# Kernel tuning notes

Measured on AMD Instinct MI355X. Metric: run time of the kernel, lower is better.

The kernel has to match this reference:

```python
import jax, jax.numpy as jnp
import numpy as np

N_NODES = 50000

def _gat_conv(x, src, dst, W, a_src, a_dst, bias, num_nodes, concat, neg_slope=0.2):
    # x: [N, Fin]; W: [Fin, H*C]; a_src/a_dst: [H, C]; src/dst: [E]
    H, C = a_src.shape
    h = (x @ W).reshape(-1, H, C)                      # [N, H, C]
    alpha_s = jnp.einsum('nhc,hc->nh', h, a_src)        # [N, H]
    alpha_d = jnp.einsum('nhc,hc->nh', h, a_dst)        # [N, H]
    e = alpha_s[src] + alpha_d[dst]                     # [E, H]
    e = jax.nn.leaky_relu(e, neg_slope)
    # segment softmax over destination nodes
    m = jax.ops.segment_max(e, dst, num_segments=num_nodes)   # [N, H]
    ex = jnp.exp(e - m[dst])                                   # [E, H]
    denom = jax.ops.segment_sum(ex, dst, num_segments=num_nodes)  # [N, H]
    alpha = ex / denom[dst]                                    # [E, H]
    msg = h[src] * alpha[:, :, None]                            # [E, H, C]
    out = jax.ops.segment_sum(msg, dst, num_segments=num_nodes)  # [N, H, C]
    if concat:
        out = out.reshape(-1, H * C)
    else:
        out = out.mean(axis=1)
    return out + bias

def _add_self_loops(edge_index, num_nodes):
    loop = jnp.arange(num_nodes, dtype=edge_index.dtype)
    src = jnp.concatenate([edge_index[0], loop])
    dst = jnp.concatenate([edge_index[1], loop])
    return src, dst

def setup_inputs() -> dict:
    key = jax.random.key(0)
    ks = jax.random.split(key, 12)
    N, E = N_NODES, 800000
    in_c, hid, out_c, H = 128, 32, 64, 4
    x = jax.random.normal(ks[0], (N, in_c), dtype=jnp.float32)
    edge_index = jax.random.randint(ks[1], (2, E), 0, N, dtype=jnp.int64)
    edge_weight = jax.random.uniform(ks[2], (E,), dtype=jnp.float32)
    s1 = 1.0 / np.sqrt(in_c)
    s2 = 1.0 / np.sqrt(hid * H)
    W1 = jax.random.normal(ks[3], (in_c, H * hid), dtype=jnp.float32) * s1
    a_src1 = jax.random.normal(ks[4], (H, hid), dtype=jnp.float32) * s1
    a_dst1 = jax.random.normal(ks[5], (H, hid), dtype=jnp.float32) * s1
    b1 = jnp.zeros((H * hid,), dtype=jnp.float32)
    W2 = jax.random.normal(ks[6], (H * hid, out_c), dtype=jnp.float32) * s2
    a_src2 = jax.random.normal(ks[7], (1, out_c), dtype=jnp.float32) * s2
    a_dst2 = jax.random.normal(ks[8], (1, out_c), dtype=jnp.float32) * s2
    b2 = jnp.zeros((out_c,), dtype=jnp.float32)
    return {"x": x, "edge_index": edge_index, "edge_weight": edge_weight,
            "W1": W1, "a_src1": a_src1, "a_dst1": a_dst1, "b1": b1,
            "W2": W2, "a_src2": a_src2, "a_dst2": a_dst2, "b2": b2}

def reference(x, edge_index, edge_weight, W1, a_src1, a_dst1, b1, W2, a_src2, a_dst2, b2):
    # PyG GATConv with edge_dim unset ignores edge_weight; self-loops added by default
    N = x.shape[0]
    src, dst = _add_self_loops(edge_index, N)
    h = _gat_conv(x, src, dst, W1, a_src1, a_dst1, b1, N, concat=True)
    h = jax.nn.relu(h)
    out = _gat_conv(h, src, dst, W2, a_src2, a_dst2, b2, N, concat=False)
    return out
```

## Files before the change

kernel.cpp:

```cpp
#include <hip/hip_runtime.h>
#include <hip/hip_fp16.h>
#include <math.h>


#define NEG_SLOPE 0.2f
#define NBLKA 256
#define MAXNB 512

__device__ __forceinline__ float leaky(float v) { return v > 0.f ? v : NEG_SLOPE * v; }

__global__ __launch_bounds__(256) void histc_k(const int* __restrict__ ei, int E, int ET,
                                               int* __restrict__ blkpref, int NB) {
  __shared__ int lhist[MAXNB];
  int chunk = (ET + NBLKA - 1) / NBLKA;
  int e0 = blockIdx.x * chunk, e1 = min(ET, e0 + chunk);
  for (int b = threadIdx.x; b < NB; b += 256) lhist[b] = 0;
  __syncthreads();
  for (int e = e0 + threadIdx.x; e < e1; e += 256) {
    int d = (e < E) ? ei[E + e] : (e - E);
    atomicAdd(&lhist[d >> 7], 1);
  }
  __syncthreads();
  for (int b = threadIdx.x; b < NB; b += 256)
    blkpref[b * NBLKA + blockIdx.x] = lhist[b];
}

__global__ __launch_bounds__(256) void scan_blk_k(int* __restrict__ blkpref,
                                                  int* __restrict__ bbase) {
  __shared__ int sm[NBLKA];
  int b = blockIdx.x, t = threadIdx.x;
  int v = blkpref[b * NBLKA + t];
  sm[t] = v;
  __syncthreads();
  #pragma unroll
  for (int off = 1; off < NBLKA; off <<= 1) {
    int x = (t >= off) ? sm[t - off] : 0;
    __syncthreads();
    sm[t] += x;
    __syncthreads();
  }
  blkpref[b * NBLKA + t] = sm[t] - v;
  if (t == NBLKA - 1) bbase[b] = sm[t];
}

__global__ __launch_bounds__(512) void scan_bkt_k(int* __restrict__ bbase,
                                                  int* __restrict__ lcnt,
                                                  int* __restrict__ rowptr,
                                                  int NB, int N, int ET) {
  __shared__ int sm[512];
  int t = threadIdx.x;
  int v = (t < NB) ? bbase[t] : 0;
  sm[t] = v;
  __syncthreads();
  #pragma unroll
  for (int off = 1; off < 512; off <<= 1) {
    int x = (t >= off) ? sm[t - off] : 0;
    __syncthreads();
    sm[t] += x;
    __syncthreads();
  }
  int excl = sm[t] - v;
  if (t <= NB) bbase[t] = excl;
  if (t == 0) { lcnt[0] = 0; lcnt[16] = 0; rowptr[N] = ET; }
}

__global__ __launch_bounds__(256) void passA_k(const int* __restrict__ ei, int E, int ET,
                                               const int* __restrict__ bbase,
                                               const int* __restrict__ blkpref,
                                               int* __restrict__ pairs, int NB) {
  __shared__ int lcur[MAXNB];
  int chunk = (ET + NBLKA - 1) / NBLKA;
  int e0 = blockIdx.x * chunk, e1 = min(ET, e0 + chunk);
  for (int b = threadIdx.x; b < NB; b += 256)
    lcur[b] = bbase[b] + blkpref[b * NBLKA + blockIdx.x];
  __syncthreads();
  for (int e = e0 + threadIdx.x; e < e1; e += 256) {
    int s, d;
    if (e < E) { s = ei[e]; d = ei[E + e]; } else { s = d = e - E; }
    int b = d >> 7;
    int pos = atomicAdd(&lcur[b], 1);
    pairs[pos] = ((d & 127) << 17) | s;
  }
}

__global__ __launch_bounds__(256) void passB_k(const int* __restrict__ pairs,
                                               const int* __restrict__ bbase,
                                               int* __restrict__ rowptr,
                                               int* __restrict__ srcs,
                                               int* __restrict__ small_list,
                                               int* __restrict__ big_list,
                                               int* __restrict__ lcnt, int N) {
  __shared__ int ncnt[128], spre[128], lcur[128];
  __shared__ int wcS[2], wcB[2], bS, bB;
  int b = blockIdx.x, t = threadIdx.x;
  int nb0 = b << 7;
  int nn = min(128, N - nb0);
  int e0 = bbase[b], e1 = bbase[b + 1];
  if (t < 128) ncnt[t] = 0;
  __syncthreads();
  for (int r = e0 + t; r < e1; r += 256)
    atomicAdd(&ncnt[pairs[r] >> 17], 1);
  __syncthreads();
  if (t < 128) spre[t] = ncnt[t];
  __syncthreads();
  #pragma unroll
  for (int off = 1; off < 128; off <<= 1) {
    int x = (t < 128 && t >= off) ? spre[t - off] : 0;
    __syncthreads();
    if (t < 128) spre[t] += x;
    __syncthreads();
  }
  if (t < nn) {
    int base = e0 + spre[t] - ncnt[t];
    rowptr[nb0 + t] = base;
    lcur[t] = base;
  }
  __syncthreads();
  for (int r = e0 + t; r < e1; r += 256) {
    int p = pairs[r];
    int pos = atomicAdd(&lcur[p >> 17], 1);
    srcs[pos] = p & 0x1FFFF;
  }
  int lane = t & 63, wv = t >> 6;
  bool valid = (t < nn);
  int deg = valid ? ncnt[t] : 0;
  bool isS = valid && (deg <= 16);
  bool isB = valid && (deg > 16);
  unsigned long long ms = __ballot(isS);
  unsigned long long mb = __ballot(isB);
  if (lane == 0 && wv < 2) { wcS[wv] = __popcll(ms); wcB[wv] = __popcll(mb); }
  __syncthreads();
  if (t == 0) {
    bS = atomicAdd(&lcnt[0],  wcS[0] + wcS[1]);
    bB = atomicAdd(&lcnt[16], wcB[0] + wcB[1]);
  }
  __syncthreads();
  unsigned long long below = (lane == 0) ? 0ull : (~0ull >> (64 - lane));
  int offS = bS + ((wv == 1) ? wcS[0] : 0);
  int offB = bB + ((wv == 1) ? wcB[0] : 0);
  if (isS) small_list[offS + __popcll(ms & below)] = nb0 + t;
  if (isB) big_list[offB + __popcll(mb & below)]   = nb0 + t;
}

__global__ __launch_bounds__(256) void gemm1_k(const float* __restrict__ X,
                                               const float* __restrict__ W,
                                               const float* __restrict__ aw_s,
                                               const float* __restrict__ aw_d,
                                               __half* __restrict__ Hh,
                                               float* __restrict__ as,
                                               float* __restrict__ ad, int N) {
  __shared__ float wl[32 * 128];
  __shared__ float xt[32][72];
  int cl = threadIdx.x & 31, rg = threadIdx.x >> 5;
  int c4 = cl * 4;
  int n0 = blockIdx.x * 64;
  float acc[8][4] = {};
  const float4* X4 = (const float4*)X;
  const float4* W4 = (const float4*)W;
  for (int k0 = 0; k0 < 128; k0 += 32) {
    __syncthreads();
    for (int i = threadIdx.x; i < 1024; i += 256)
      ((float4*)wl)[i] = W4[k0 * 32 + i];
    for (int i = threadIdx.x; i < 512; i += 256) {
      int r = i >> 3, kk4 = (i & 7) * 4;
      int n = n0 + r;
      float4 xv = (n < N) ? X4[(size_t)n * 32 + (k0 >> 2) + (i & 7)]
                          : make_float4(0.f, 0.f, 0.f, 0.f);
      xt[kk4 + 0][r] = xv.x; xt[kk4 + 1][r] = xv.y;
      xt[kk4 + 2][r] = xv.z; xt[kk4 + 3][r] = xv.w;
    }
    __syncthreads();
    #pragma unroll 8
    for (int kk = 0; kk < 32; ++kk) {
      float4 w4 = *(const float4*)&wl[kk * 128 + c4];
      float4 xa = *(const float4*)&xt[kk][rg * 8];
      float4 xb = *(const float4*)&xt[kk][rg * 8 + 4];
      float xr[8] = {xa.x, xa.y, xa.z, xa.w, xb.x, xb.y, xb.z, xb.w};
      #pragma unroll
      for (int j = 0; j < 8; ++j) {
        acc[j][0] += xr[j] * w4.x; acc[j][1] += xr[j] * w4.y;
        acc[j][2] += xr[j] * w4.z; acc[j][3] += xr[j] * w4.w;
      }
    }
  }
  float4 aws = *(const float4*)&aw_s[c4];
  float4 awd = *(const float4*)&aw_d[c4];
  #pragma unroll
  for (int j = 0; j < 8; ++j) {
    int n = n0 + rg * 8 + j;
    float ps = acc[j][0] * aws.x + acc[j][1] * aws.y + acc[j][2] * aws.z + acc[j][3] * aws.w;
    float pd = acc[j][0] * awd.x + acc[j][1] * awd.y + acc[j][2] * awd.z + acc[j][3] * awd.w;
    ps += __shfl_xor(ps, 1); ps += __shfl_xor(ps, 2); ps += __shfl_xor(ps, 4);
    pd += __shfl_xor(pd, 1); pd += __shfl_xor(pd, 2); pd += __shfl_xor(pd, 4);
    if (n < N) {
      __half2* dst = (__half2*)&Hh[(size_t)n * 128 + c4];
      dst[0] = __floats2half2_rn(acc[j][0], acc[j][1]);
      dst[1] = __floats2half2_rn(acc[j][2], acc[j][3]);
      if ((cl & 7) == 0) {
        as[n * 4 + (cl >> 3)] = ps;
        ad[n * 4 + (cl >> 3)] = pd;
      }
    }
  }
}

__global__ __launch_bounds__(256) void gemm2_k(const __half* __restrict__ X,
                                               const float* __restrict__ W,
                                               const float* __restrict__ aw_s,
                                               const float* __restrict__ aw_d,
                                               __half* __restrict__ Hh,
                                               float* __restrict__ as,
                                               float* __restrict__ ad, int N) {
  __shared__ float wl[32 * 64];
  __shared__ float xt[32][72];
  int cl = threadIdx.x & 15, rg = threadIdx.x >> 4;
  int c4 = cl * 4;
  int n0 = blockIdx.x * 64;
  float acc[4][4] = {};
  const uint4* X8 = (const uint4*)X;
  const float4* W4 = (const float4*)W;
  for (int k0 = 0; k0 < 128; k0 += 32) {
    __syncthreads();
    for (int i = threadIdx.x; i < 512; i += 256)
      ((float4*)wl)[i] = W4[k0 * 16 + i];
    for (int i = threadIdx.x; i < 256; i += 256) {
      int r = i >> 2, kk8 = (i & 3) * 8;
      int n = n0 + r;
      uint4 hv = (n < N) ? X8[(size_t)n * 16 + (k0 >> 3) + (i & 3)]
                         : make_uint4(0, 0, 0, 0);
      float2 f0 = __half22float2(*(const __half2*)&hv.x);
      float2 f1 = __half22float2(*(const __half2*)&hv.y);
      float2 f2 = __half22float2(*(const __half2*)&hv.z);
      float2 f3 = __half22float2(*(const __half2*)&hv.w);
      xt[kk8 + 0][r] = f0.x; xt[kk8 + 1][r] = f0.y;
      xt[kk8 + 2][r] = f1.x; xt[kk8 + 3][r] = f1.y;
      xt[kk8 + 4][r] = f2.x; xt[kk8 + 5][r] = f2.y;
      xt[kk8 + 6][r] = f3.x; xt[kk8 + 7][r] = f3.y;
    }
    __syncthreads();
    #pragma unroll 8
    for (int kk = 0; kk < 32; ++kk) {
      float4 w4 = *(const float4*)&wl[kk * 64 + c4];
      float4 xa = *(const float4*)&xt[kk][rg * 4];
      float xr[4] = {xa.x, xa.y, xa.z, xa.w};
      #pragma unroll
      for (int j = 0; j < 4; ++j) {
        acc[j][0] += xr[j] * w4.x; acc[j][1] += xr[j] * w4.y;
        acc[j][2] += xr[j] * w4.z; acc[j][3] += xr[j] * w4.w;
      }
    }
  }
  float4 aws = *(const float4*)&aw_s[c4];
  float4 awd = *(const float4*)&aw_d[c4];
  #pragma unroll
  for (int j = 0; j < 4; ++j) {
    int n = n0 + rg * 4 + j;
    float ps = acc[j][0] * aws.x + acc[j][1] * aws.y + acc[j][2] * aws.z + acc[j][3] * aws.w;
    float pd = acc[j][0] * awd.x + acc[j][1] * awd.y + acc[j][2] * awd.z + acc[j][3] * awd.w;
    ps += __shfl_xor(ps, 1); ps += __shfl_xor(ps, 2);
    ps += __shfl_xor(ps, 4); ps += __shfl_xor(ps, 8);
    pd += __shfl_xor(pd, 1); pd += __shfl_xor(pd, 2);
    pd += __shfl_xor(pd, 4); pd += __shfl_xor(pd, 8);
    if (n < N) {
      __half2* dst = (__half2*)&Hh[(size_t)n * 64 + c4];
      dst[0] = __floats2half2_rn(acc[j][0], acc[j][1]);
      dst[1] = __floats2half2_rn(acc[j][2], acc[j][3]);
      if (cl == 0) { as[n] = ps; ad[n] = pd; }
    }
  }
}

__device__ __forceinline__ void load8h(const __half* p, float* f) {
  uint4 hv = *(const uint4*)p;
  float2 f0 = __half22float2(*(const __half2*)&hv.x);
  float2 f1 = __half22float2(*(const __half2*)&hv.y);
  float2 f2 = __half22float2(*(const __half2*)&hv.z);
  float2 f3 = __half22float2(*(const __half2*)&hv.w);
  f[0] = f0.x; f[1] = f0.y; f[2] = f1.x; f[3] = f1.y;
  f[4] = f2.x; f[5] = f2.y; f[6] = f3.x; f[7] = f3.y;
}

__global__ __launch_bounds__(256) void agg1_k(const int* __restrict__ rowptr,
                                              const int* __restrict__ srcs,
                                              const float* __restrict__ as,
                                              const float* __restrict__ ad,
                                              const __half* __restrict__ Hm,
                                              const float* __restrict__ bias,
                                              __half* __restrict__ out,
                                              const int* __restrict__ small_list,
                                              const int* __restrict__ big_list,
                                              const int* __restrict__ lcnt, int SB) {
  if (blockIdx.x < (unsigned)SB) {
    __shared__ float al_sm[16][17][4];
    __shared__ int   sr_sm[16][16];
    int g  = threadIdx.x >> 4;
    int gl = threadIdx.x & 15;
    int gidx = blockIdx.x * 16 + g;
    if (gidx >= lcnt[0]) return;
    int n = small_list[gidx];
    int r0 = rowptr[n];
    int deg = rowptr[n + 1] - r0;
    float4 adn = *(const float4*)&ad[n * 4];

    float e0 = -INFINITY, e1 = -INFINITY, e2 = -INFINITY, e3 = -INFINITY;
    int s = 0;
    if (gl < deg) {
      s = srcs[r0 + gl];
      float4 av = *(const float4*)&as[s * 4];
      e0 = leaky(av.x + adn.x); e1 = leaky(av.y + adn.y);
      e2 = leaky(av.z + adn.z); e3 = leaky(av.w + adn.w);
    }
    sr_sm[g][gl] = s;
    float m0 = e0, m1 = e1, m2 = e2, m3 = e3;
    #pragma unroll
    for (int off = 8; off > 0; off >>= 1) {
      m0 = fmaxf(m0, __shfl_xor(m0, off, 16)); m1 = fmaxf(m1, __shfl_xor(m1, off, 16));
      m2 = fmaxf(m2, __shfl_xor(m2, off, 16)); m3 = fmaxf(m3, __shfl_xor(m3, off, 16));
    }
    float sc0 = (gl < deg) ? __expf(e0 - m0) : 0.f;
    float sc1 = (gl < deg) ? __expf(e1 - m1) : 0.f;
    float sc2 = (gl < deg) ? __expf(e2 - m2) : 0.f;
    float sc3 = (gl < deg) ? __expf(e3 - m3) : 0.f;
    float s0 = sc0, s1 = sc1, s2 = sc2, s3 = sc3;
    #pragma unroll
    for (int off = 8; off > 0; off >>= 1) {
      s0 += __shfl_xor(s0, off, 16); s1 += __shfl_xor(s1, off, 16);
      s2 += __shfl_xor(s2, off, 16); s3 += __shfl_xor(s3, off, 16);
    }
    *(float4*)&al_sm[g][gl][0] =
        make_float4(sc0 / s0, sc1 / s1, sc2 / s2, sc3 / s3);

    int h = gl >> 2;
    int cbase = gl * 8;
    float a0 = 0.f, a1 = 0.f, a2 = 0.f, a3 = 0.f,
          a4 = 0.f, a5 = 0.f, a6 = 0.f, a7 = 0.f;
    for (int j = 0; j < deg; j += 4) {
      #pragma unroll
      for (int u = 0; u < 4; ++u) {
        int idx = j + u;
        bool vU = idx < deg;
        int jj = vU ? idx : 0;
        int   sU  = sr_sm[g][jj];
        float alU = vU ? al_sm[g][jj][h] : 0.f;
        float f[8];
        load8h(&Hm[(size_t)sU * 128 + cbase], f);
        a0 += f[0] * alU; a1 += f[1] * alU; a2 += f[2] * alU; a3 += f[3] * alU;
        a4 += f[4] * alU; a5 += f[5] * alU; a6 += f[6] * alU; a7 += f[7] * alU;
      }
    }
    float4 b0 = *(const float4*)&bias[cbase];
    float4 b1 = *(const float4*)&bias[cbase + 4];
    __half2* dst = (__half2*)&out[(size_t)n * 128 + cbase];
    dst[0] = __floats2half2_rn(fmaxf(a0 + b0.x, 0.f), fmaxf(a1 + b0.y, 0.f));
    dst[1] = __floats2half2_rn(fmaxf(a2 + b0.z, 0.f), fmaxf(a3 + b0.w, 0.f));
    dst[2] = __floats2half2_rn(fmaxf(a4 + b1.x, 0.f), fmaxf(a5 + b1.y, 0.f));
    dst[3] = __floats2half2_rn(fmaxf(a6 + b1.z, 0.f), fmaxf(a7 + b1.w, 0.f));
    return;
  }
  __shared__ float al_sm[4][64][4];
  __shared__ int   sr_sm[4][64];
  int wv = threadIdx.x >> 6, lane = threadIdx.x & 63;
  int widx = (blockIdx.x - SB) * 4 + wv;
  if (widx >= lcnt[16]) return;
  int n = big_list[widx];
  int r0 = rowptr[n], r1 = rowptr[n + 1];
  int deg = r1 - r0;
  int grp = lane >> 4, gl = lane & 15, h = gl >> 2;
  int cbase = gl * 8;
  float4 adn = *(const float4*)&ad[n * 4];

  float a0 = 0.f, a1 = 0.f, a2 = 0.f, a3 = 0.f,
        a4 = 0.f, a5 = 0.f, a6 = 0.f, a7 = 0.f;

  if (deg <= 64) {
    float e0 = -INFINITY, e1 = -INFINITY, e2 = -INFINITY, e3 = -INFINITY;
    int s = 0;
    if (lane < deg) {
      s = srcs[r0 + lane];
      float4 av = *(const float4*)&as[s * 4];
      e0 = leaky(av.x + adn.x); e1 = leaky(av.y + adn.y);
      e2 = leaky(av.z + adn.z); e3 = leaky(av.w + adn.w);
    }
    sr_sm[wv][lane] = s;
    float m0 = e0, m1 = e1, m2 = e2, m3 = e3;
    #pragma unroll
    for (int off = 32; off > 0; off >>= 1) {
      m0 = fmaxf(m0, __shfl_xor(m0, off)); m1 = fmaxf(m1, __shfl_xor(m1, off));
      m2 = fmaxf(m2, __shfl_xor(m2, off)); m3 = fmaxf(m3, __shfl_xor(m3, off));
    }
    float sc0 = (lane < deg) ? __expf(e0 - m0) : 0.f;
    float sc1 = (lane < deg) ? __expf(e1 - m1) : 0.f;
    float sc2 = (lane < deg) ? __expf(e2 - m2) : 0.f;
    float sc3 = (lane < deg) ? __expf(e3 - m3) : 0.f;
    float s0 = sc0, s1 = sc1, s2 = sc2, s3 = sc3;
    #pragma unroll
    for (int off = 32; off > 0; off >>= 1) {
      s0 += __shfl_xor(s0, off); s1 += __shfl_xor(s1, off);
      s2 += __shfl_xor(s2, off); s3 += __shfl_xor(s3, off);
    }
    *(float4*)&al_sm[wv][lane][0] =
        make_float4(sc0 / s0, sc1 / s1, sc2 / s2, sc3 / s3);

    for (int base = 0; base < deg; base += 16) {
      #pragma unroll
      for (int u = 0; u < 4; ++u) {
        int idx = base + grp * 4 + u;
        bool vU = idx < deg;
        int jj = vU ? idx : 0;
        int   sU  = sr_sm[wv][jj];
        float alU = vU ? al_sm[wv][jj][h] : 0.f;
        float f[8];
        load8h(&Hm[(size_t)sU * 128 + cbase], f);
        a0 += f[0] * alU; a1 += f[1] * alU; a2 += f[2] * alU; a3 += f[3] * alU;
        a4 += f[4] * alU; a5 += f[5] * alU; a6 += f[6] * alU; a7 += f[7] * alU;
      }
    }
  } else {
    float m0 = -INFINITY, m1 = -INFINITY, m2 = -INFINITY, m3 = -INFINITY;
    for (int r = r0 + lane; r < r1; r += 64) {
      int s = srcs[r];
      float4 av = *(const float4*)&as[s * 4];
      m0 = fmaxf(m0, leaky(av.x + adn.x)); m1 = fmaxf(m1, leaky(av.y + adn.y));
      m2 = fmaxf(m2, leaky(av.z + adn.z)); m3 = fmaxf(m3, leaky(av.w + adn.w));
    }
    #pragma unroll
    for (int off = 32; off > 0; off >>= 1) {
      m0 = fmaxf(m0, __shfl_xor(m0, off)); m1 = fmaxf(m1, __shfl_xor(m1, off));
      m2 = fmaxf(m2, __shfl_xor(m2, off)); m3 = fmaxf(m3, __shfl_xor(m3, off));
    }
    float s0 = 0.f, s1 = 0.f, s2 = 0.f, s3 = 0.f;
    for (int r = r0 + lane; r < r1; r += 64) {
      int s = srcs[r];
      float4 av = *(const float4*)&as[s * 4];
      s0 += __expf(leaky(av.x + adn.x) - m0); s1 += __expf(leaky(av.y + adn.y) - m1);
      s2 += __expf(leaky(av.z + adn.z) - m2); s3 += __expf(leaky(av.w + adn.w) - m3);
    }
    #pragma unroll
    for (int off = 32; off > 0; off >>= 1) {
      s0 += __shfl_xor(s0, off); s1 += __shfl_xor(s1, off);
      s2 += __shfl_xor(s2, off); s3 += __shfl_xor(s3, off);
    }
    float mhh = (h == 0) ? m0 : (h == 1) ? m1 : (h == 2) ? m2 : m3;
    float inv = 1.f / ((h == 0) ? s0 : (h == 1) ? s1 : (h == 2) ? s2 : s3);
    float adh = (h == 0) ? adn.x : (h == 1) ? adn.y : (h == 2) ? adn.z : adn.w;
    for (int r = r0; r < r1; r += 8) {
      int rA = r + grp, rB = rA + 4;
      bool vA = rA < r1, vB = rB < r1;
      int sA = srcs[vA ? rA : r0];
      int sB = srcs[vB ? rB : r0];
      float avA = as[sA * 4 + h], avB = as[sB * 4 + h];
      float alA = vA ? (__expf(leaky(avA + adh) - mhh) * inv) : 0.f;
      float alB = vB ? (__expf(leaky(avB + adh) - mhh) * inv) : 0.f;
      float fA[8], fB[8];
      load8h(&Hm[(size_t)sA * 128 + cbase], fA);
      load8h(&Hm[(size_t)sB * 128 + cbase], fB);
      a0 += fA[0] * alA + fB[0] * alB; a1 += fA[1] * alA + fB[1] * alB;
      a2 += fA[2] * alA + fB[2] * alB; a3 += fA[3] * alA + fB[3] * alB;
      a4 += fA[4] * alA + fB[4] * alB; a5 += fA[5] * alA + fB[5] * alB;
      a6 += fA[6] * alA + fB[6] * alB; a7 += fA[7] * alA + fB[7] * alB;
    }
  }
  a0 += __shfl_xor(a0, 16); a0 += __shfl_xor(a0, 32);
  a1 += __shfl_xor(a1, 16); a1 += __shfl_xor(a1, 32);
  a2 += __shfl_xor(a2, 16); a2 += __shfl_xor(a2, 32);
  a3 += __shfl_xor(a3, 16); a3 += __shfl_xor(a3, 32);
  a4 += __shfl_xor(a4, 16); a4 += __shfl_xor(a4, 32);
  a5 += __shfl_xor(a5, 16); a5 += __shfl_xor(a5, 32);
  a6 += __shfl_xor(a6, 16); a6 += __shfl_xor(a6, 32);
  a7 += __shfl_xor(a7, 16); a7 += __shfl_xor(a7, 32);
  if (grp == 0) {
    float4 b0 = *(const float4*)&bias[cbase];
    float4 b1 = *(const float4*)&bias[cbase + 4];
    __half2* dst = (__half2*)&out[(size_t)n * 128 + cbase];
    dst[0] = __floats2half2_rn(fmaxf(a0 + b0.x, 0.f), fmaxf(a1 + b0.y, 0.f));
    dst[1] = __floats2half2_rn(fmaxf(a2 + b0.z, 0.f), fmaxf(a3 + b0.w, 0.f));
    dst[2] = __floats2half2_rn(fmaxf(a4 + b1.x, 0.f), fmaxf(a5 + b1.y, 0.f));
    dst[3] = __floats2half2_rn(fmaxf(a6 + b1.z, 0.f), fmaxf(a7 + b1.w, 0.f));
  }
}

__global__ __launch_bounds__(256) void agg2_k(const int* __restrict__ rowptr,
                                              const int* __restrict__ srcs,
                                              const float* __restrict__ as,
                                              const float* __restrict__ ad,
                                              const __half* __restrict__ Hm,
                                              const float* __restrict__ bias,
                                              float* __restrict__ out,
                                              const int* __restrict__ small_list,
                                              const int* __restrict__ big_list,
                                              const int* __restrict__ lcnt, int SB) {
  if (blockIdx.x < (unsigned)SB) {
    __shared__ float al_sm[16][17];
    __shared__ int   sr_sm[16][16];
    int g  = threadIdx.x >> 4;
    int gl = threadIdx.x & 15;
    int gidx = blockIdx.x * 16 + g;
    if (gidx >= lcnt[0]) return;
    int n = small_list[gidx];
    int r0 = rowptr[n];
    int deg = rowptr[n + 1] - r0;
    float adn = ad[n];

    float e = -INFINITY;
    int s = 0;
    if (gl < deg) { s = srcs[r0 + gl]; e = leaky(as[s] + adn); }
    sr_sm[g][gl] = s;
    float m = e;
    #pragma unroll
    for (int off = 8; off > 0; off >>= 1) m = fmaxf(m, __shfl_xor(m, off, 16));
    float sc = (gl < deg) ? __expf(e - m) : 0.f;
    float ssum = sc;
    #pragma unroll
    for (int off = 8; off > 0; off >>= 1) ssum += __shfl_xor(ssum, off, 16);
    al_sm[g][gl] = sc / ssum;

    int cbase = gl * 4;
    float a0 = 0.f, a1 = 0.f, a2 = 0.f, a3 = 0.f;
    for (int j = 0; j < deg; j += 4) {
      #pragma unroll
      for (int u = 0; u < 4; ++u) {
        int idx = j + u;
        bool vU = idx < deg;
        int jj = vU ? idx : 0;
        int   sU  = sr_sm[g][jj];
        float alU = vU ? al_sm[g][jj] : 0.f;
        uint2 hv = *(const uint2*)&Hm[(size_t)sU * 64 + cbase];
        float2 f0 = __half22float2(*(const __half2*)&hv.x);
        float2 f1 = __half22float2(*(const __half2*)&hv.y);
        a0 += f0.x * alU; a1 += f0.y * alU; a2 += f1.x * alU; a3 += f1.y * alU;
      }
    }
    float4 bv = *(const float4*)&bias[cbase];
    float4 o;
    o.x = a0 + bv.x; o.y = a1 + bv.y; o.z = a2 + bv.z; o.w = a3 + bv.w;
    *(float4*)&out[(size_t)n * 64 + cbase] = o;
    return;
  }
  __shared__ float al_sm[4][64];
  __shared__ int   sr_sm[4][64];
  int wv = threadIdx.x >> 6, lane = threadIdx.x & 63;
  int widx = (blockIdx.x - SB) * 4 + wv;
  if (widx >= lcnt[16]) return;
  int n = big_list[widx];
  int r0 = rowptr[n], r1 = rowptr[n + 1];
  int deg = r1 - r0;
  int grp = lane >> 4, gl = lane & 15;
  int cbase = gl * 4;
  float adn = ad[n];

  float a0 = 0.f, a1 = 0.f, a2 = 0.f, a3 = 0.f;

  if (deg <= 64) {
    float e = -INFINITY;
    int s = 0;
    if (lane < deg) { s = srcs[r0 + lane]; e = leaky(as[s] + adn); }
    sr_sm[wv][lane] = s;
    float m = e;
    #pragma unroll
    for (int off = 32; off > 0; off >>= 1) m = fmaxf(m, __shfl_xor(m, off));
    float sc = (lane < deg) ? __expf(e - m) : 0.f;
    float ssum = sc;
    #pragma unroll
    for (int off = 32; off > 0; off >>= 1) ssum += __shfl_xor(ssum, off);
    al_sm[wv][lane] = sc / ssum;

    for (int base = 0; base < deg; base += 16) {
      #pragma unroll
      for (int u = 0; u < 4; ++u) {
        int idx = base + grp * 4 + u;
        bool vU = idx < deg;
        int jj = vU ? idx : 0;
        int   sU  = sr_sm[wv][jj];
        float alU = vU ? al_sm[wv][jj] : 0.f;
        uint2 hv = *(const uint2*)&Hm[(size_t)sU * 64 + cbase];
        float2 f0 = __half22float2(*(const __half2*)&hv.x);
        float2 f1 = __half22float2(*(const __half2*)&hv.y);
        a0 += f0.x * alU; a1 += f0.y * alU; a2 += f1.x * alU; a3 += f1.y * alU;
      }
    }
  } else {
    float mh = -INFINITY;
    for (int r = r0 + lane; r < r1; r += 64)
      mh = fmaxf(mh, leaky(as[srcs[r]] + adn));
    #pragma unroll
    for (int off = 32; off > 0; off >>= 1) mh = fmaxf(mh, __shfl_xor(mh, off));
    float ssum = 0.f;
    for (int r = r0 + lane; r < r1; r += 64)
      ssum += __expf(leaky(as[srcs[r]] + adn) - mh);
    #pragma unroll
    for (int off = 32; off > 0; off >>= 1) ssum += __shfl_xor(ssum, off);
    float inv = 1.f / ssum;
    for (int r = r0; r < r1; r += 8) {
      int rA = r + grp, rB = rA + 4;
      bool vA = rA < r1, vB = rB < r1;
      int sA = srcs[vA ? rA : r0];
      int sB = srcs[vB ? rB : r0];
      float alA = vA ? (__expf(leaky(as[sA] + adn) - mh) * inv) : 0.f;
      float alB = vB ? (__expf(leaky(as[sB] + adn) - mh) * inv) : 0.f;
      uint2 hvA = *(const uint2*)&Hm[(size_t)sA * 64 + cbase];
      uint2 hvB = *(const uint2*)&Hm[(size_t)sB * 64 + cbase];
      float2 fA0 = __half22float2(*(const __half2*)&hvA.x);
      float2 fA1 = __half22float2(*(const __half2*)&hvA.y);
      float2 fB0 = __half22float2(*(const __half2*)&hvB.x);
      float2 fB1 = __half22float2(*(const __half2*)&hvB.y);
      a0 += fA0.x * alA + fB0.x * alB; a1 += fA0.y * alA + fB0.y * alB;
      a2 += fA1.x * alA + fB1.x * alB; a3 += fA1.y * alA + fB1.y * alB;
    }
  }
  a0 += __shfl_xor(a0, 16); a0 += __shfl_xor(a0, 32);
  a1 += __shfl_xor(a1, 16); a1 += __shfl_xor(a1, 32);
  a2 += __shfl_xor(a2, 16); a2 += __shfl_xor(a2, 32);
  a3 += __shfl_xor(a3, 16); a3 += __shfl_xor(a3, 32);
  if (grp == 0) {
    float4 bv = *(const float4*)&bias[cbase];
    float4 o;
    o.x = a0 + bv.x; o.y = a1 + bv.y; o.z = a2 + bv.z; o.w = a3 + bv.w;
    *(float4*)&out[(size_t)n * 64 + cbase] = o;
  }
}

extern "C" void kernel_launch(void* const* d_in, const int* in_sizes, int n_in,
                              void* d_out, int out_size, void* d_ws, size_t ws_size,
                              hipStream_t stream) {
  const float* x   = (const float*)d_in[0];
  const int*   ei  = (const int*)d_in[1];
  const float* W1  = (const float*)d_in[3];
  const float* aS1 = (const float*)d_in[4];
  const float* aD1 = (const float*)d_in[5];
  const float* b1  = (const float*)d_in[6];
  const float* W2  = (const float*)d_in[7];
  const float* aS2 = (const float*)d_in[8];
  const float* aD2 = (const float*)d_in[9];
  const float* b2  = (const float*)d_in[10];

  const int N  = in_sizes[0] / 128;
  const int E  = in_sizes[2];
  const int ET = E + N;
  const int NB = (N + 127) >> 7;

  float* ws    = (float*)d_ws;
  __half* h1h  = (__half*)ws;
  __half* o1h  = (__half*)(ws + (size_t)N * 64);
  float* as1   = ws + (size_t)N * 128;
  float* ad1   = as1  + (size_t)4 * N;
  float* as2   = ad1  + (size_t)4 * N;
  float* ad2   = as2  + (size_t)N;
  int*   lcnt    = (int*)(ad2 + (size_t)N);
  int*   rowptr  = lcnt + 32;
  int*   bbase   = rowptr + N + 1;
  int*   blkpref = bbase + NB + 1;
  int*   small_list = blkpref + NB * NBLKA;
  int*   big_list   = small_list + N;
  int*   srcs   = big_list + N;
  int*   pairs  = (int*)ws;
  __half* h2h  = h1h;
  float* out  = (float*)d_out;

  const int gb = (N + 63) / 64;
  const int sb = (N + 15) / 16;
  const int bb = (N + 3) / 4;

  histc_k<<<NBLKA, 256, 0, stream>>>(ei, E, ET, blkpref, NB);
  scan_blk_k<<<NB, 256, 0, stream>>>(blkpref, bbase);
  scan_bkt_k<<<1, 512, 0, stream>>>(bbase, lcnt, rowptr, NB, N, ET);
  passA_k<<<NBLKA, 256, 0, stream>>>(ei, E, ET, bbase, blkpref, pairs, NB);
  passB_k<<<NB, 256, 0, stream>>>(pairs, bbase, rowptr, srcs,
                                  small_list, big_list, lcnt, N);

  gemm1_k<<<gb, 256, 0, stream>>>(x, W1, aS1, aD1, h1h, as1, ad1, N);
  agg1_k<<<sb + bb, 256, 0, stream>>>(rowptr, srcs, as1, ad1, h1h, b1, o1h,
                                      small_list, big_list, lcnt, sb);

  gemm2_k<<<gb, 256, 0, stream>>>(o1h, W2, aS2, aD2, h2h, as2, ad2, N);
  agg2_k<<<sb + bb, 256, 0, stream>>>(rowptr, srcs, as2, ad2, h2h, b2, out,
                                      small_list, big_list, lcnt, sb);
}
```

Before: 231.8 us.

## Use fp16 MFMA for both GAT projection GEMMs with pre-transposed weights

Replaces the scalar FP32 FMA tiling in both projection GEMMs with 16x16x32 fp16 MFMA instructions. Operands are staged in padded LDS tiles, and the weights are transposed and converted to fp16 once inside the histogram kernel. The attention logits are now computed from the fp16-rounded outputs read back from LDS. This is meant to cut GEMM compute time, at the cost of fp16 rounding of X in layer 1 and more LDS traffic.

Result: faster. 216.4 us (-6.7%).

```diff
diff --git a/kernel.cpp b/kernel.cpp
--- a/kernel.cpp
+++ b/kernel.cpp
@@ -6,11 +6,19 @@
 #define NEG_SLOPE 0.2f
 #define NBLKA 256
 #define MAXNB 512
+#define LDH 136
+
+typedef _Float16 f16x8 __attribute__((ext_vector_type(8)));
+typedef float f32x4 __attribute__((ext_vector_type(4)));
 
 __device__ __forceinline__ float leaky(float v) { return v > 0.f ? v : NEG_SLOPE * v; }
 
 __global__ __launch_bounds__(256) void histc_k(const int* __restrict__ ei, int E, int ET,
-                                               int* __restrict__ blkpref, int NB) {
+                                               int* __restrict__ blkpref, int NB,
+                                               const float* __restrict__ W1,
+                                               const float* __restrict__ W2,
+                                               _Float16* __restrict__ w1t,
+                                               _Float16* __restrict__ w2t) {
   __shared__ int lhist[MAXNB];
   int chunk = (ET + NBLKA - 1) / NBLKA;
   int e0 = blockIdx.x * chunk, e1 = min(ET, e0 + chunk);
@@ -23,6 +31,25 @@
   __syncthreads();
   for (int b = threadIdx.x; b < NB; b += 256)
     blkpref[b * NBLKA + blockIdx.x] = lhist[b];
+  if (blockIdx.x == 0) {
+    int t = threadIdx.x;
+    if (t < 128) {
+      union { _Float16 h[8]; uint4 u; } buf;
+      for (int k0 = 0; k0 < 128; k0 += 8) {
+        #pragma unroll
+        for (int u = 0; u < 8; ++u) buf.h[u] = (_Float16)W1[(k0 + u) * 128 + t];
+        *(uint4*)&w1t[t * 128 + k0] = buf.u;
+      }
+    } else if (t < 192) {
+      int n = t - 128;
+      union { _Float16 h[8]; uint4 u; } buf;
+      for (int k0 = 0; k0 < 128; k0 += 8) {
+        #pragma unroll
+        for (int u = 0; u < 8; ++u) buf.h[u] = (_Float16)W2[(k0 + u) * 64 + n];
+        *(uint4*)&w2t[n * 128 + k0] = buf.u;
+      }
+    }
+  }
 }
 
 __global__ __launch_bounds__(256) void scan_blk_k(int* __restrict__ blkpref,
@@ -143,130 +170,154 @@
 }
 
 __global__ __launch_bounds__(256) void gemm1_k(const float* __restrict__ X,
-                                               const float* __restrict__ W,
+                                               const _Float16* __restrict__ WT,
                                                const float* __restrict__ aw_s,
                                                const float* __restrict__ aw_d,
                                                __half* __restrict__ Hh,
                                                float* __restrict__ as,
                                                float* __restrict__ ad, int N) {
-  __shared__ float wl[32 * 128];
-  __shared__ float xt[32][72];
-  int cl = threadIdx.x & 31, rg = threadIdx.x >> 5;
-  int c4 = cl * 4;
+  __shared__ _Float16 xs[64 * LDH];
+  __shared__ _Float16 wt[128 * LDH];
+  int t = threadIdx.x;
   int n0 = blockIdx.x * 64;
-  float acc[8][4] = {};
-  const float4* X4 = (const float4*)X;
-  const float4* W4 = (const float4*)W;
-  for (int k0 = 0; k0 < 128; k0 += 32) {
-    __syncthreads();
-    for (int i = threadIdx.x; i < 1024; i += 256)
-      ((float4*)wl)[i] = W4[k0 * 32 + i];
-    for (int i = threadIdx.x; i < 512; i += 256) {
-      int r = i >> 3, kk4 = (i & 7) * 4;
-      int n = n0 + r;
-      float4 xv = (n < N) ? X4[(size_t)n * 32 + (k0 >> 2) + (i & 7)]
-                          : make_float4(0.f, 0.f, 0.f, 0.f);
-      xt[kk4 + 0][r] = xv.x; xt[kk4 + 1][r] = xv.y;
-      xt[kk4 + 2][r] = xv.z; xt[kk4 + 3][r] = xv.w;
-    }
-    __syncthreads();
-    #pragma unroll 8
-    for (int kk = 0; kk < 32; ++kk) {
-      float4 w4 = *(const float4*)&wl[kk * 128 + c4];
-      float4 xa = *(const float4*)&xt[kk][rg * 8];
-      float4 xb = *(const float4*)&xt[kk][rg * 8 + 4];
-      float xr[8] = {xa.x, xa.y, xa.z, xa.w, xb.x, xb.y, xb.z, xb.w};
-      #pragma unroll
-      for (int j = 0; j < 8; ++j) {
-        acc[j][0] += xr[j] * w4.x; acc[j][1] += xr[j] * w4.y;
-        acc[j][2] += xr[j] * w4.z; acc[j][3] += xr[j] * w4.w;
-      }
-    }
-  }
-  float4 aws = *(const float4*)&aw_s[c4];
-  float4 awd = *(const float4*)&aw_d[c4];
+  for (int i = t; i < 2048; i += 256) {
+    int r = i >> 4, c8 = i & 15;
+    *(uint4*)&wt[r * LDH + c8 * 8] = ((const uint4*)WT)[i];
+  }
+  for (int i = t; i < 2048; i += 256) {
+    int r = i >> 5, c4 = i & 31;
+    int n = n0 + r;
+    float4 xv = (n < N) ? ((const float4*)X)[(size_t)n * 32 + c4]
+                        : make_float4(0.f, 0.f, 0.f, 0.f);
+    __half2 h0 = __floats2half2_rn(xv.x, xv.y);
+    __half2 h1 = __floats2half2_rn(xv.z, xv.w);
+    uint2 u; u.x = *(unsigned*)&h0; u.y = *(unsigned*)&h1;
+    *(uint2*)&xs[r * LDH + c4 * 4] = u;
+  }
+  __syncthreads();
+  int wv = t >> 6, l = t & 63;
+  int row16 = l & 15, kg = l >> 4;
+  f32x4 acc[8];
+  #pragma unroll
+  for (int j = 0; j < 8; ++j) acc[j] = (f32x4){0.f, 0.f, 0.f, 0.f};
+  #pragma unroll
+  for (int kk = 0; kk < 4; ++kk) {
+    int kbase = kk * 32 + kg * 8;
+    f16x8 afr = *(f16x8*)&xs[(wv * 16 + row16) * LDH + kbase];
+    #pragma unroll
+    for (int j = 0; j < 8; ++j) {
+      f16x8 bfr = *(f16x8*)&wt[(j * 16 + row16) * LDH + kbase];
+      acc[j] = __builtin_amdgcn_mfma_f32_16x16x32_f16(afr, bfr, acc[j], 0, 0, 0);
+    }
+  }
+  __syncthreads();
   #pragma unroll
   for (int j = 0; j < 8; ++j) {
-    int n = n0 + rg * 8 + j;
-    float ps = acc[j][0] * aws.x + acc[j][1] * aws.y + acc[j][2] * aws.z + acc[j][3] * aws.w;
-    float pd = acc[j][0] * awd.x + acc[j][1] * awd.y + acc[j][2] * awd.z + acc[j][3] * awd.w;
-    ps += __shfl_xor(ps, 1); ps += __shfl_xor(ps, 2); ps += __shfl_xor(ps, 4);
-    pd += __shfl_xor(pd, 1); pd += __shfl_xor(pd, 2); pd += __shfl_xor(pd, 4);
-    if (n < N) {
-      __half2* dst = (__half2*)&Hh[(size_t)n * 128 + c4];
-      dst[0] = __floats2half2_rn(acc[j][0], acc[j][1]);
-      dst[1] = __floats2half2_rn(acc[j][2], acc[j][3]);
-      if ((cl & 7) == 0) {
-        as[n * 4 + (cl >> 3)] = ps;
-        ad[n * 4 + (cl >> 3)] = pd;
-      }
-    }
+    int col = j * 16 + row16;
+    #pragma unroll
+    for (int r = 0; r < 4; ++r) {
+      int row = wv * 16 + kg * 4 + r;
+      xs[row * LDH + col] = (_Float16)acc[j][r];
+    }
+  }
+  __syncthreads();
+  for (int i = t; i < 1024; i += 256) {
+    int r = i >> 4, c8 = i & 15;
+    int n = n0 + r;
+    if (n < N) ((uint4*)Hh)[(size_t)n * 16 + c8] = *(uint4*)&xs[r * LDH + c8 * 8];
+  }
+  {
+    int r = t >> 2, h = t & 3;
+    int n = n0 + r;
+    float ps = 0.f, pd = 0.f;
+    #pragma unroll
+    for (int q = 0; q < 4; ++q) {
+      f16x8 hv = *(f16x8*)&xs[r * LDH + h * 32 + q * 8];
+      float4 s0 = *(const float4*)&aw_s[h * 32 + q * 8];
+      float4 s1 = *(const float4*)&aw_s[h * 32 + q * 8 + 4];
+      float4 d0 = *(const float4*)&aw_d[h * 32 + q * 8];
+      float4 d1 = *(const float4*)&aw_d[h * 32 + q * 8 + 4];
+      ps += (float)hv[0] * s0.x + (float)hv[1] * s0.y + (float)hv[2] * s0.z + (float)hv[3] * s0.w
+          + (float)hv[4] * s1.x + (float)hv[5] * s1.y + (float)hv[6] * s1.z + (float)hv[7] * s1.w;
+      pd += (float)hv[0] * d0.x + (float)hv[1] * d0.y + (float)hv[2] * d0.z + (float)hv[3] * d0.w
+          + (float)hv[4] * d1.x + (float)hv[5] * d1.y + (float)hv[6] * d1.z + (float)hv[7] * d1.w;
+    }
+    if (n < N) { as[n * 4 + h] = ps; ad[n * 4 + h] = pd; }
   }
 }
 
 __global__ __launch_bounds__(256) void gemm2_k(const __half* __restrict__ X,
-                                               const float* __restrict__ W,
+                                               const _Float16* __restrict__ WT,
                                                const float* __restrict__ aw_s,
                                                const float* __restrict__ aw_d,
                                                __half* __restrict__ Hh,
                                                float* __restrict__ as,
                                                float* __restrict__ ad, int N) {
-  __shared__ float wl[32 * 64];
-  __shared__ float xt[32][72];
-  int cl = threadIdx.x & 15, rg = threadIdx.x >> 4;
-  int c4 = cl * 4;
+  __shared__ _Float16 xs[64 * LDH];
+  __shared__ _Float16 wt[64 * LDH];
+  int t = threadIdx.x;
   int n0 = blockIdx.x * 64;
-  float acc[4][4] = {};
-  const uint4* X8 = (const uint4*)X;
-  const float4* W4 = (const float4*)W;
-  for (int k0 = 0; k0 < 128; k0 += 32) {
-    __syncthreads();
-    for (int i = threadIdx.x; i < 512; i += 256)
-      ((float4*)wl)[i] = W4[k0 * 16 + i];
-    for (int i = threadIdx.x; i < 256; i += 256) {
-      int r = i >> 2, kk8 = (i & 3) * 8;
-      int n = n0 + r;
-      uint4 hv = (n < N) ? X8[(size_t)n * 16 + (k0 >> 3) + (i & 3)]
-                         : make_uint4(0, 0, 0, 0);
-      float2 f0 = __half22float2(*(const __half2*)&hv.x);
-      float2 f1 = __half22float2(*(const __half2*)&hv.y);
-      float2 f2 = __half22float2(*(const __half2*)&hv.z);
-      float2 f3 = __half22float2(*(const __half2*)&hv.w);
-      xt[kk8 + 0][r] = f0.x; xt[kk8 + 1][r] = f0.y;
-      xt[kk8 + 2][r] = f1.x; xt[kk8 + 3][r] = f1.y;
-      xt[kk8 + 4][r] = f2.x; xt[kk8 + 5][r] = f2.y;
-      xt[kk8 + 6][r] = f3.x; xt[kk8 + 7][r] = f3.y;
-    }
-    __syncthreads();
-    #pragma unroll 8
-    for (int kk = 0; kk < 32; ++kk) {
-      float4 w4 = *(const float4*)&wl[kk * 64 + c4];
-      float4 xa = *(const float4*)&xt[kk][rg * 4];
-      float xr[4] = {xa.x, xa.y, xa.z, xa.w};
-      #pragma unroll
-      for (int j = 0; j < 4; ++j) {
-        acc[j][0] += xr[j] * w4.x; acc[j][1] += xr[j] * w4.y;
-        acc[j][2] += xr[j] * w4.z; acc[j][3] += xr[j] * w4.w;
-      }
-    }
-  }
-  float4 aws = *(const float4*)&aw_s[c4];
-  float4 awd = *(const float4*)&aw_d[c4];
+  for (int i = t; i < 1024; i += 256) {
+    int r = i >> 4, c8 = i & 15;
+    *(uint4*)&wt[r * LDH + c8 * 8] = ((const uint4*)WT)[i];
+  }
+  for (int i = t; i < 1024; i += 256) {
+    int r = i >> 4, c8 = i & 15;
+    int n = n0 + r;
+    uint4 v = (n < N) ? ((const uint4*)X)[(size_t)n * 16 + c8] : make_uint4(0, 0, 0, 0);
+    *(uint4*)&xs[r * LDH + c8 * 8] = v;
+  }
+  __syncthreads();
+  int wv = t >> 6, l = t & 63;
+  int row16 = l & 15, kg = l >> 4;
+  f32x4 acc[4];
+  #pragma unroll
+  for (int j = 0; j < 4; ++j) acc[j] = (f32x4){0.f, 0.f, 0.f, 0.f};
+  #pragma unroll
+  for (int kk = 0; kk < 4; ++kk) {
+    int kbase = kk * 32 + kg * 8;
+    f16x8 afr = *(f16x8*)&xs[(wv * 16 + row16) * LDH + kbase];
+    #pragma unroll
+    for (int j = 0; j < 4; ++j) {
+      f16x8 bfr = *(f16x8*)&wt[(j * 16 + row16) * LDH + kbase];
+      acc[j] = __builtin_amdgcn_mfma_f32_16x16x32_f16(afr, bfr, acc[j], 0, 0, 0);
+    }
+  }
+  __syncthreads();
   #pragma unroll
   for (int j = 0; j < 4; ++j) {
-    int n = n0 + rg * 4 + j;
-    float ps = acc[j][0] * aws.x + acc[j][1] * aws.y + acc[j][2] * aws.z + acc[j][3] * aws.w;
-    float pd = acc[j][0] * awd.x + acc[j][1] * awd.y + acc[j][2] * awd.z + acc[j][3] * awd.w;
+    int col = j * 16 + row16;
+    #pragma unroll
+    for (int r = 0; r < 4; ++r) {
+      int row = wv * 16 + kg * 4 + r;
+      xs[row * LDH + col] = (_Float16)acc[j][r];
+    }
+  }
+  __syncthreads();
+  for (int i = t; i < 512; i += 256) {
+    int r = i >> 3, c8 = i & 7;
+    int n = n0 + r;
+    if (n < N) ((uint4*)Hh)[(size_t)n * 8 + c8] = *(uint4*)&xs[r * LDH + c8 * 8];
+  }
+  {
+    int r = t >> 2, q = t & 3;
+    int n = n0 + r;
+    float ps = 0.f, pd = 0.f;
+    #pragma unroll
+    for (int qq = 0; qq < 2; ++qq) {
+      f16x8 hv = *(f16x8*)&xs[r * LDH + q * 16 + qq * 8];
+      float4 s0 = *(const float4*)&aw_s[q * 16 + qq * 8];
+      float4 s1 = *(const float4*)&aw_s[q * 16 + qq * 8 + 4];
+      float4 d0 = *(const float4*)&aw_d[q * 16 + qq * 8];
+      float4 d1 = *(const float4*)&aw_d[q * 16 + qq * 8 + 4];
+      ps += (float)hv[0] * s0.x + (float)hv[1] * s0.y + (float)hv[2] * s0.z + (float)hv[3] * s0.w
+          + (float)hv[4] * s1.x + (float)hv[5] * s1.y + (float)hv[6] * s1.z + (float)hv[7] * s1.w;
+      pd += (float)hv[0] * d0.x + (float)hv[1] * d0.y + (float)hv[2] * d0.z + (float)hv[3] * d0.w
+          + (float)hv[4] * d1.x + (float)hv[5] * d1.y + (float)hv[6] * d1.z + (float)hv[7] * d1.w;
+    }
     ps += __shfl_xor(ps, 1); ps += __shfl_xor(ps, 2);
-    ps += __shfl_xor(ps, 4); ps += __shfl_xor(ps, 8);
     pd += __shfl_xor(pd, 1); pd += __shfl_xor(pd, 2);
-    pd += __shfl_xor(pd, 4); pd += __shfl_xor(pd, 8);
-    if (n < N) {
-      __half2* dst = (__half2*)&Hh[(size_t)n * 64 + c4];
-      dst[0] = __floats2half2_rn(acc[j][0], acc[j][1]);
-      dst[1] = __floats2half2_rn(acc[j][2], acc[j][3]);
-      if (cl == 0) { as[n] = ps; ad[n] = pd; }
-    }
+    if (q == 0 && n < N) { as[n] = ps; ad[n] = pd; }
   }
 }
 
@@ -652,6 +703,8 @@
   int*   small_list = blkpref + NB * NBLKA;
   int*   big_list   = small_list + N;
   int*   srcs   = big_list + N;
+  _Float16* w1t = (_Float16*)(srcs + ET);
+  _Float16* w2t = w1t + 128 * 128;
   int*   pairs  = (int*)ws;
   __half* h2h  = h1h;
   float* out  = (float*)d_out;
@@ -660,18 +713,18 @@
   const int sb = (N + 15) / 16;
   const int bb = (N + 3) / 4;
 
-  histc_k<<<NBLKA, 256, 0, stream>>>(ei, E, ET, blkpref, NB);
+  histc_k<<<NBLKA, 256, 0, stream>>>(ei, E, ET, blkpref, NB, W1, W2, w1t, w2t);
   scan_blk_k<<<NB, 256, 0, stream>>>(blkpref, bbase);
   scan_bkt_k<<<1, 512, 0, stream>>>(bbase, lcnt, rowptr, NB, N, ET);
   passA_k<<<NBLKA, 256, 0, stream>>>(ei, E, ET, bbase, blkpref, pairs, NB);
   passB_k<<<NB, 256, 0, stream>>>(pairs, bbase, rowptr, srcs,
                                   small_list, big_list, lcnt, N);
 
-  gemm1_k<<<gb, 256, 0, stream>>>(x, W1, aS1, aD1, h1h, as1, ad1, N);
+  gemm1_k<<<gb, 256, 0, stream>>>(x, w1t, aS1, aD1, h1h, as1, ad1, N);
   agg1_k<<<sb + bb, 256, 0, stream>>>(rowptr, srcs, as1, ad1, h1h, b1, o1h,
                                       small_list, big_list, lcnt, sb);
 
-  gemm2_k<<<gb, 256, 0, stream>>>(o1h, W2, aS2, aD2, h2h, as2, ad2, N);
+  gemm2_k<<<gb, 256, 0, stream>>>(o1h, w2t, aS2, aD2, h2h, as2, ad2, N);
   agg2_k<<<sb + bb, 256, 0, stream>>>(rowptr, srcs, as2, ad2, h2h, b2, out,
                                       small_list, big_list, lcnt, sb);
 }
```
